# Optimization experiments

Measured on AMD Instinct MI355X. Metric: run time of the kernel, lower is better.

Reference implementation:

```python
import jax, jax.numpy as jnp
import numpy as np

B, N, F, K = 16384, 64, 128, 64


def setup_inputs() -> dict:
    key = jax.random.key(0)
    kx, kd = jax.random.split(key)
    x = jax.random.normal(kx, (B, F), dtype=jnp.float32)
    D = jax.random.normal(kd, (N, F, K), dtype=jnp.float32)  # per-cluster factor dictionaries
    return {"x": x, "D": D}


def reference(x, D):
    # --- assignment step (torch.no_grad in original) ---
    # Dtx[n,b,j] = sum_i D[n,i,j] * x[b,i]
    Dtx = jnp.einsum('nij,bi->nbj', D, x)                      # [N,B,K]
    # per-cluster (D^T D)^{-1}, batched inverse over the cluster axis
    DTD = jnp.einsum('nij,nik->njk', D, D)                     # [N,K,K]
    DTD_inv = jnp.linalg.inv(DTD)                              # [N,K,K]
    Cs = jnp.einsum('nbj,nkj->nbk', Dtx, DTD_inv)              # [N,B,K]
    x_hat = jnp.einsum('nij,nbj->nbi', D, Cs)                  # [N,B,F]
    # nearest-subspace assignment per sample
    label = jnp.argmin(jnp.linalg.norm(x_hat - x[None], axis=-1), axis=0)  # [B] int
    C = Cs[label, jnp.arange(x.shape[0])]                      # [B,K] gather per sample
    # --- reconstruction loss: sum_i || x[i] - D[label[i]] @ C[i] ||^2 ---
    x_rec = jnp.einsum('bik,bk->bi', D[label], C)              # grouped gather + matmul
    se_loss = jnp.sum(jnp.square(x - x_rec))
    return se_loss, label
```

## Files before the change

### kernel.cpp

```cpp
#include <hip/hip_runtime.h>
#include <hip/hip_bf16.h>

#define B_N 16384
#define TAU 0.25f
#define GS 68
#define YS 133

typedef float f32x4 __attribute__((ext_vector_type(4)));
typedef short s16x8 __attribute__((ext_vector_type(8)));

__device__ __forceinline__ void gl_lds16(const void* g, void* l) {
    __builtin_amdgcn_global_load_lds(
        (const __attribute__((address_space(1))) void*)g,
        (__attribute__((address_space(3))) void*)l, 16, 0, 0);
}

__device__ __forceinline__ unsigned short bf16_bits(float v) {
    __hip_bfloat16 h = __float2bfloat16(v);
    return *reinterpret_cast<unsigned short*>(&h);
}

__global__ __launch_bounds__(256) void prep_convert(const float* __restrict__ x,
                                                    const float* __restrict__ D,
                                                    unsigned short* __restrict__ xh,
                                                    float* __restrict__ nrm,
                                                    float* __restrict__ Qg,
                                                    unsigned short* __restrict__ Bht,
                                                    float* __restrict__ out) {
    const int t = threadIdx.x;

    if (blockIdx.x >= 64) {
        const int gid = (blockIdx.x - 64) * 256 + t;
        if (gid == 0) out[0] = 0.0f;
        const size_t base = (size_t)gid * 32;
        float s = 0.0f;
        #pragma unroll
        for (int c = 0; c < 8; ++c) {
            const f32x4 v = ((const f32x4*)(x + base))[c];
            s += v.x * v.x + v.y * v.y + v.z * v.z + v.w * v.w;
            ushort4 h;
            h.x = bf16_bits(v.x); h.y = bf16_bits(v.y);
            h.z = bf16_bits(v.z); h.w = bf16_bits(v.w);
            ((ushort4*)(xh + base))[c] = h;
        }
        s += __shfl_xor(s, 1, 64);
        s += __shfl_xor(s, 2, 64);
        if ((gid & 3) == 0) nrm[gid >> 2] = s;
        return;
    }

    __shared__ float Y[64 * YS];
    __shared__ __align__(16) float G[64 * GS + 64];
    __shared__ __align__(16) float Lti[8 * 8 * 8];
    const int n = blockIdx.x;
    const float* Dn = D + (size_t)n * 8192;

    for (int e4 = t; e4 < 2048; e4 += 256) {
        const int c = e4 >> 4, j4 = (e4 & 15) * 4;
        const f32x4 v = ((const f32x4*)Dn)[e4];
        Y[(j4 + 0) * YS + c] = v.x;
        Y[(j4 + 1) * YS + c] = v.y;
        Y[(j4 + 2) * YS + c] = v.z;
        Y[(j4 + 3) * YS + c] = v.w;
    }

    {
        const int a0 = (t & 15) * 4, b0 = (t >> 4) * 4;
        float acc[4][4] = {};
        #pragma unroll 4
        for (int i = 0; i < 128; ++i) {
            const f32x4 av = *(const f32x4*)(Dn + i * 64 + a0);
            const f32x4 bv = *(const f32x4*)(Dn + i * 64 + b0);
            const float aa[4] = {av.x, av.y, av.z, av.w};
            const float bb[4] = {bv.x, bv.y, bv.z, bv.w};
            #pragma unroll
            for (int p = 0; p < 4; ++p)
                #pragma unroll
                for (int q = 0; q < 4; ++q) acc[p][q] = fmaf(aa[p], bb[q], acc[p][q]);
        }
        #pragma unroll
        for (int p = 0; p < 4; ++p)
            #pragma unroll
            for (int q = 0; q < 4; ++q) G[(a0 + p) * GS + b0 + q] = acc[p][q];
    }
    __syncthreads();

    for (int p8 = 0; p8 < 8; ++p8) {
        const int pb = p8 * 8;
        if (t < 64) {
            const int lane = t;
            const f32x4 v0 = *(const f32x4*)&G[lane * GS + pb];
            const f32x4 v1 = *(const f32x4*)&G[lane * GS + pb + 4];
            float g[8] = {v0.x, v0.y, v0.z, v0.w, v1.x, v1.y, v1.z, v1.w};
            #pragma unroll
            for (int kk = 0; kk < 8; ++kk) {
                const int k = pb + kk;
                const float dk = __shfl(g[kk], k, 64);
                const float rinv = 1.0f / sqrtf(dk);
                const float lik = g[kk] * rinv;
                g[kk] = lik;
                if (lane == 0) G[64 * GS + k] = rinv;
                #pragma unroll
                for (int jj = kk + 1; jj < 8; ++jj) {
                    const float ljk = __shfl(lik, pb + jj, 64);
                    g[jj] -= lik * ljk;
                }
            }
            *(f32x4*)&G[lane * GS + pb]     = (f32x4){g[0], g[1], g[2], g[3]};
            *(f32x4*)&G[lane * GS + pb + 4] = (f32x4){g[4], g[5], g[6], g[7]};
        }
        __syncthreads();
        const int base = pb + 8;
        if (base < 64) {
            for (int i = base + (t >> 5); i < 64; i += 8) {
                const f32x4 Li0 = *(const f32x4*)&G[i * GS + pb];
                const f32x4 Li1 = *(const f32x4*)&G[i * GS + pb + 4];
                for (int j = base + (t & 31); j < 64; j += 32) {
                    const f32x4 Lj0 = *(const f32x4*)&G[j * GS + pb];
                    const f32x4 Lj1 = *(const f32x4*)&G[j * GS + pb + 4];
                    float s = G[i * GS + j];
                    s -= Li0.x * Lj0.x + Li0.y * Lj0.y + Li0.z * Lj0.z + Li0.w * Lj0.w;
                    s -= Li1.x * Lj1.x + Li1.y * Lj1.y + Li1.z * Lj1.z + Li1.w * Lj1.w;
                    G[i * GS + j] = s;
                }
            }
        }
        __syncthreads();
    }

    if (t < 64) {
        const int bi = t >> 3, c = t & 7;
        const int base = bi * 8;
        float m[8];
        #pragma unroll
        for (int r = 0; r < 8; ++r) {
            float s = (r == c) ? 1.0f : 0.0f;
            #pragma unroll
            for (int k = 0; k < r; ++k)
                s -= G[(base + r) * GS + base + k] * m[k];
            m[r] = s * G[64 * GS + base + r];
        }
        #pragma unroll
        for (int r = 0; r < 8; ++r) Lti[(base + r) * 8 + c] = m[r];
    }
    __syncthreads();

    if (t < 128) {
        const int c = t;
        for (int i = 0; i < 8; ++i) {
            float Tv[8];
            #pragma unroll
            for (int r = 0; r < 8; ++r) Tv[r] = Y[(i * 8 + r) * YS + c];
            for (int k = 0; k < i; ++k) {
                #pragma unroll
                for (int kk = 0; kk < 8; ++kk) {
                    const float z = Y[(k * 8 + kk) * YS + c];
                    #pragma unroll
                    for (int r = 0; r < 8; ++r)
                        Tv[r] -= G[(i * 8 + r) * GS + k * 8 + kk] * z;
                }
            }
            #pragma unroll
            for (int r = 0; r < 8; ++r) {
                float z = 0.0f;
                #pragma unroll
                for (int rp = 0; rp <= r; ++rp)
                    z += Lti[(i * 8 + r) * 8 + rp] * Tv[rp];
                Y[(i * 8 + r) * YS + c] = z;
            }
        }
    }
    __syncthreads();

    for (int e = t; e < 8192; e += 256) {
        const int j = e >> 7, i = e & 127;
        Bht[((size_t)n * 64 + j) * 128 + i] = bf16_bits(Y[j * YS + i]);
    }
    for (int e = t; e < 8192; e += 256) {
        const int i = e >> 6, j = e & 63;
        Qg[(size_t)n * 8192 + e] = Y[j * YS + i];
    }
}

__global__ __launch_bounds__(256) void gemm_argmax(const unsigned short* __restrict__ xh,
                                                   const unsigned short* __restrict__ Bht,
                                                   const float* __restrict__ nrm,
                                                   const float* __restrict__ x,
                                                   const float* __restrict__ Qg,
                                                   float* __restrict__ out) {
    __shared__ __align__(16) unsigned short ldsA[64 * 128];
    __shared__ float scL[64 * 65];
    __shared__ float mrg[4][64][3];
    __shared__ int sflags[64];
    __shared__ int scnt;
    __shared__ float ssum;
    __shared__ float scorr[4];

    const int t = threadIdx.x, w = t >> 6, lane = t & 63;
    const int m0 = blockIdx.x * 64;
    const int lm = lane & 15, lg = lane >> 4;
    if (t == 0) scnt = 0;
    if (t < 4) scorr[t] = 0.0f;

    {
        const int rl = lane >> 4, sp = lane & 15;
        #pragma unroll
        for (int q = 0; q < 4; ++q) {
            const int row = w * 16 + q * 4 + rl;
            const int c = sp ^ (row & 15);
            gl_lds16(xh + (size_t)(m0 + row) * 128 + c * 8,
                     &ldsA[(w * 16 + q * 4) * 128]);
        }
    }
    __syncthreads();

    s16x8 bfr[4][4];
    #pragma unroll
    for (int st = 0; st < 4; ++st) {
        const int r = st * 16 + lm;
        #pragma unroll
        for (int ks = 0; ks < 4; ++ks) {
            const int p = (ks * 4 + lg) ^ (r & 15);
            bfr[st][ks] = *(const s16x8*)&ldsA[r * 128 + p * 8];
        }
    }

    float v1[4] = {-1e30f, -1e30f, -1e30f, -1e30f};
    float v2[4] = {-1e30f, -1e30f, -1e30f, -1e30f};
    int   n1[4] = {0, 0, 0, 0};

    const unsigned short* afbase = Bht + (size_t)lm * 128 + lg * 8;

#define LOAD_AF(dst, cc) do {                                                   \
    const unsigned short* bp = afbase + (size_t)(cc) * 8192;                    \
    _Pragma("unroll")                                                           \
    for (int mt_ = 0; mt_ < 4; ++mt_)                                           \
        _Pragma("unroll")                                                       \
        for (int ks_ = 0; ks_ < 4; ++ks_)                                       \
            dst[mt_][ks_] = *(const s16x8*)(bp + mt_ * 2048 + ks_ * 32);        \
} while (0)

#define PROC(af, cc) do {                                                       \
    _Pragma("unroll")                                                           \
    for (int st_ = 0; st_ < 4; ++st_) {                                         \
        f32x4 ac0 = {0.f,0.f,0.f,0.f}, ac1 = {0.f,0.f,0.f,0.f};                 \
        f32x4 ac2 = {0.f,0.f,0.f,0.f}, ac3 = {0.f,0.f,0.f,0.f};                 \
        _Pragma("unroll")                                                       \
        for (int ks_ = 0; ks_ < 4; ++ks_) {                                     \
            ac0 = __builtin_amdgcn_mfma_f32_16x16x32_bf16(af[0][ks_], bfr[st_][ks_], ac0, 0, 0, 0); \
            ac1 = __builtin_amdgcn_mfma_f32_16x16x32_bf16(af[1][ks_], bfr[st_][ks_], ac1, 0, 0, 0); \
            ac2 = __builtin_amdgcn_mfma_f32_16x16x32_bf16(af[2][ks_], bfr[st_][ks_], ac2, 0, 0, 0); \
            ac3 = __builtin_amdgcn_mfma_f32_16x16x32_bf16(af[3][ks_], bfr[st_][ks_], ac3, 0, 0, 0); \
        }                                                                       \
        float q0 = ac0[0]*ac0[0]; q0 = fmaf(ac0[1],ac0[1],q0);                  \
        q0 = fmaf(ac0[2],ac0[2],q0); q0 = fmaf(ac0[3],ac0[3],q0);               \
        float q1 = ac1[0]*ac1[0]; q1 = fmaf(ac1[1],ac1[1],q1);                  \
        q1 = fmaf(ac1[2],ac1[2],q1); q1 = fmaf(ac1[3],ac1[3],q1);               \
        float q2 = ac2[0]*ac2[0]; q2 = fmaf(ac2[1],ac2[1],q2);                  \
        q2 = fmaf(ac2[2],ac2[2],q2); q2 = fmaf(ac2[3],ac2[3],q2);               \
        float q3 = ac3[0]*ac3[0]; q3 = fmaf(ac3[1],ac3[1],q3);                  \
        q3 = fmaf(ac3[2],ac3[2],q3); q3 = fmaf(ac3[3],ac3[3],q3);               \
        float s_ = ((q0 + q1) + q2) + q3;                                       \
        s_ += __shfl_xor(s_, 16, 64);                                           \
        s_ += __shfl_xor(s_, 32, 64);                                           \
        if (lg == 0) scL[(st_ * 16 + lm) * 65 + (cc)] = s_;                     \
        if (s_ > v1[st_]) { v2[st_] = v1[st_]; v1[st_] = s_; n1[st_] = (cc); }  \
        else v2[st_] = fmaxf(v2[st_], s_);                                      \
    }                                                                           \
} while (0)

    {
        const int cb = w * 16;
        s16x8 afA[4][4], afB[4][4];
        LOAD_AF(afA, cb);
        #pragma unroll 1
        for (int ci = 0; ci < 16; ci += 2) {
            LOAD_AF(afB, cb + ci + 1);
            PROC(afA, cb + ci);
            if (ci < 14) LOAD_AF(afA, cb + ci + 2);
            PROC(afB, cb + ci + 1);
        }
    }
#undef LOAD_AF
#undef PROC

    if (lg == 0) {
        #pragma unroll
        for (int st = 0; st < 4; ++st) {
            mrg[w][st * 16 + lm][0] = v1[st];
            mrg[w][st * 16 + lm][1] = v2[st];
            mrg[w][st * 16 + lm][2] = (float)n1[st];
        }
    }
    __syncthreads();

    if (t < 64) {
        float b1 = -1e30f, b2 = -1e30f;
        int bn = 0;
        #pragma unroll
        for (int ww = 0; ww < 4; ++ww) {
            const float a1 = mrg[ww][t][0];
            const float a2 = mrg[ww][t][1];
            const int an = (int)mrg[ww][t][2];
            if (a1 > b1) { b2 = fmaxf(b1, a2); b1 = a1; bn = an; }
            else b2 = fmaxf(b2, a1);
        }
        out[1 + m0 + t] = (float)bn;
        if (b1 - b2 < TAU) { const int i = atomicAdd(&scnt, 1); sflags[i] = t; }
        float err = nrm[m0 + t] - b1;
        err += __shfl_xor(err, 1, 64);
        err += __shfl_xor(err, 2, 64);
        err += __shfl_xor(err, 4, 64);
        err += __shfl_xor(err, 8, 64);
        err += __shfl_xor(err, 16, 64);
        err += __shfl_xor(err, 32, 64);
        if (t == 0) ssum = err;
    }
    __syncthreads();

    const int nf = scnt;
    float corr = 0.0f;
    for (int f = w; f < nf; f += 4) {
        const int s = sflags[f];
        const int b2 = m0 + s;
        const float v = scL[s * 65 + lane];
        float vm = v;
        for (int off = 32; off; off >>= 1) vm = fmaxf(vm, __shfl_xor(vm, off, 64));
        unsigned long long mask = __ballot((vm - v) < TAU);
        float best = -1e30f;
        int bn = 0;
        while (mask) {
            const int nn = (int)__builtin_ctzll(mask);
            mask &= mask - 1;
            const float* Qn = Qg + (size_t)nn * 8192;
            const float* xb = x + (size_t)b2 * 128;
            float d0 = 0.0f, d1 = 0.0f, d2 = 0.0f, d3 = 0.0f;
            #pragma unroll
            for (int i = 0; i < 128; i += 4) {
                d0 = fmaf(Qn[(i + 0) * 64 + lane], xb[i + 0], d0);
                d1 = fmaf(Qn[(i + 1) * 64 + lane], xb[i + 1], d1);
                d2 = fmaf(Qn[(i + 2) * 64 + lane], xb[i + 2], d2);
                d3 = fmaf(Qn[(i + 3) * 64 + lane], xb[i + 3], d3);
            }
            const float dot = (d0 + d1) + (d2 + d3);
            float sv = dot * dot;
            for (int off = 32; off; off >>= 1) sv += __shfl_xor(sv, off, 64);
            if (sv > best) { best = sv; bn = nn; }
        }
        if (lane == 0) {
            out[1 + b2] = (float)bn;
            corr += vm - best;
        }
    }
    if (lane == 0 && corr != 0.0f) scorr[w] += corr;
    __syncthreads();
    if (t == 0)
        atomicAdd(out, ssum + scorr[0] + scorr[1] + scorr[2] + scorr[3]);
}

extern "C" void kernel_launch(void* const* d_in, const int* in_sizes, int n_in,
                              void* d_out, int out_size, void* d_ws, size_t ws_size,
                              hipStream_t stream) {
    const float* x = (const float*)d_in[0];
    const float* D = (const float*)d_in[1];
    float* out = (float*)d_out;

    char* ws = (char*)d_ws;
    unsigned short* xh  = (unsigned short*)(ws);
    unsigned short* Bht = (unsigned short*)(ws + (4u << 20));
    float* Qg           = (float*)(ws + (5u << 20));
    float* nrm          = (float*)(ws + (11u << 20));

    prep_convert<<<320, 256, 0, stream>>>(x, D, xh, nrm, Qg, Bht, out);
    gemm_argmax<<<256, 256, 0, stream>>>(xh, Bht, nrm, x, Qg, out);
}
```

Measured before the change: 149.3 us.

## Shrink gemm_argmax tile to 16 rows per block and launch 1024 blocks

Cuts the per-block sample tile from 64 to 16 rows and launches four times as many blocks. The goal is to fill all CUs (256 blocks underfill a 256-CU part with one block each) and to lower register and LDS use so more waves can be resident. It also drops the explicit double-buffered prefetch of the B fragments. In exchange, each B fragment loaded from global/L2 is reused across only 16 rows instead of 64, which quadruples B traffic, and there is more per-block overhead including more atomics on the output.

```diff
diff --git a/kernel.cpp b/kernel.cpp
--- a/kernel.cpp
+++ b/kernel.cpp
@@ -182,119 +182,91 @@
     }
 }
 
-__global__ __launch_bounds__(256) void gemm_argmax(const unsigned short* __restrict__ xh,
-                                                   const unsigned short* __restrict__ Bht,
-                                                   const float* __restrict__ nrm,
-                                                   const float* __restrict__ x,
-                                                   const float* __restrict__ Qg,
-                                                   float* __restrict__ out) {
-    __shared__ __align__(16) unsigned short ldsA[64 * 128];
-    __shared__ float scL[64 * 65];
-    __shared__ float mrg[4][64][3];
-    __shared__ int sflags[64];
+__global__ __launch_bounds__(256, 4) void gemm_argmax(const unsigned short* __restrict__ xh,
+                                                      const unsigned short* __restrict__ Bht,
+                                                      const float* __restrict__ nrm,
+                                                      const float* __restrict__ x,
+                                                      const float* __restrict__ Qg,
+                                                      float* __restrict__ out) {
+    __shared__ __align__(16) unsigned short ldsA[16 * 128];
+    __shared__ float scL[16 * 65];
+    __shared__ float mrg[4][16][3];
+    __shared__ int sflags[16];
     __shared__ int scnt;
     __shared__ float ssum;
     __shared__ float scorr[4];
 
     const int t = threadIdx.x, w = t >> 6, lane = t & 63;
-    const int m0 = blockIdx.x * 64;
+    const int m0 = blockIdx.x * 16;
     const int lm = lane & 15, lg = lane >> 4;
     if (t == 0) scnt = 0;
     if (t < 4) scorr[t] = 0.0f;
 
     {
         const int rl = lane >> 4, sp = lane & 15;
-        #pragma unroll
-        for (int q = 0; q < 4; ++q) {
-            const int row = w * 16 + q * 4 + rl;
-            const int c = sp ^ (row & 15);
-            gl_lds16(xh + (size_t)(m0 + row) * 128 + c * 8,
-                     &ldsA[(w * 16 + q * 4) * 128]);
-        }
-    }
-    __syncthreads();
-
-    s16x8 bfr[4][4];
+        const int row = w * 4 + rl;
+        const int c = sp ^ (row & 15);
+        gl_lds16(xh + (size_t)(m0 + row) * 128 + c * 8, &ldsA[(w * 4) * 128]);
+    }
+    __syncthreads();
+
+    s16x8 bfr[4];
     #pragma unroll
-    for (int st = 0; st < 4; ++st) {
-        const int r = st * 16 + lm;
+    for (int ks = 0; ks < 4; ++ks) {
+        const int p = (ks * 4 + lg) ^ (lm & 15);
+        bfr[ks] = *(const s16x8*)&ldsA[lm * 128 + p * 8];
+    }
+
+    float v1 = -1e30f, v2 = -1e30f;
+    int n1 = 0;
+
+    const unsigned short* afbase = Bht + (size_t)lm * 128 + lg * 8;
+
+    #pragma unroll 1
+    for (int ci = 0; ci < 16; ++ci) {
+        const int cc = w * 16 + ci;
+        const unsigned short* bp = afbase + (size_t)cc * 8192;
+
+        s16x8 af[4][4];
+        #pragma unroll
+        for (int mt = 0; mt < 4; ++mt)
+            #pragma unroll
+            for (int ks = 0; ks < 4; ++ks)
+                af[mt][ks] = *(const s16x8*)(bp + mt * 2048 + ks * 32);
+
+        f32x4 ac0 = {0.f,0.f,0.f,0.f}, ac1 = {0.f,0.f,0.f,0.f};
+        f32x4 ac2 = {0.f,0.f,0.f,0.f}, ac3 = {0.f,0.f,0.f,0.f};
         #pragma unroll
         for (int ks = 0; ks < 4; ++ks) {
-            const int p = (ks * 4 + lg) ^ (r & 15);
-            bfr[st][ks] = *(const s16x8*)&ldsA[r * 128 + p * 8];
-        }
-    }
-
-    float v1[4] = {-1e30f, -1e30f, -1e30f, -1e30f};
-    float v2[4] = {-1e30f, -1e30f, -1e30f, -1e30f};
-    int   n1[4] = {0, 0, 0, 0};
-
-    const unsigned short* afbase = Bht + (size_t)lm * 128 + lg * 8;
-
-#define LOAD_AF(dst, cc) do {                                                   \
-    const unsigned short* bp = afbase + (size_t)(cc) * 8192;                    \
-    _Pragma("unroll")                                                           \
-    for (int mt_ = 0; mt_ < 4; ++mt_)                                           \
-        _Pragma("unroll")                                                       \
-        for (int ks_ = 0; ks_ < 4; ++ks_)                                       \
-            dst[mt_][ks_] = *(const s16x8*)(bp + mt_ * 2048 + ks_ * 32);        \
-} while (0)
-
-#define PROC(af, cc) do {                                                       \
-    _Pragma("unroll")                                                           \
-    for (int st_ = 0; st_ < 4; ++st_) {                                         \
-        f32x4 ac0 = {0.f,0.f,0.f,0.f}, ac1 = {0.f,0.f,0.f,0.f};                 \
-        f32x4 ac2 = {0.f,0.f,0.f,0.f}, ac3 = {0.f,0.f,0.f,0.f};                 \
-        _Pragma("unroll")                                                       \
-        for (int ks_ = 0; ks_ < 4; ++ks_) {                                     \
-            ac0 = __builtin_amdgcn_mfma_f32_16x16x32_bf16(af[0][ks_], bfr[st_][ks_], ac0, 0, 0, 0); \
-            ac1 = __builtin_amdgcn_mfma_f32_16x16x32_bf16(af[1][ks_], bfr[st_][ks_], ac1, 0, 0, 0); \
-            ac2 = __builtin_amdgcn_mfma_f32_16x16x32_bf16(af[2][ks_], bfr[st_][ks_], ac2, 0, 0, 0); \
-            ac3 = __builtin_amdgcn_mfma_f32_16x16x32_bf16(af[3][ks_], bfr[st_][ks_], ac3, 0, 0, 0); \
-        }                                                                       \
-        float q0 = ac0[0]*ac0[0]; q0 = fmaf(ac0[1],ac0[1],q0);                  \
-        q0 = fmaf(ac0[2],ac0[2],q0); q0 = fmaf(ac0[3],ac0[3],q0);               \
-        float q1 = ac1[0]*ac1[0]; q1 = fmaf(ac1[1],ac1[1],q1);                  \
-        q1 = fmaf(ac1[2],ac1[2],q1); q1 = fmaf(ac1[3],ac1[3],q1);               \
-        float q2 = ac2[0]*ac2[0]; q2 = fmaf(ac2[1],ac2[1],q2);                  \
-        q2 = fmaf(ac2[2],ac2[2],q2); q2 = fmaf(ac2[3],ac2[3],q2);               \
-        float q3 = ac3[0]*ac3[0]; q3 = fmaf(ac3[1],ac3[1],q3);                  \
-        q3 = fmaf(ac3[2],ac3[2],q3); q3 = fmaf(ac3[3],ac3[3],q3);               \
-        float s_ = ((q0 + q1) + q2) + q3;                                       \
-        s_ += __shfl_xor(s_, 16, 64);                                           \
-        s_ += __shfl_xor(s_, 32, 64);                                           \
-        if (lg == 0) scL[(st_ * 16 + lm) * 65 + (cc)] = s_;                     \
-        if (s_ > v1[st_]) { v2[st_] = v1[st_]; v1[st_] = s_; n1[st_] = (cc); }  \
-        else v2[st_] = fmaxf(v2[st_], s_);                                      \
-    }                                                                           \
-} while (0)
-
-    {
-        const int cb = w * 16;
-        s16x8 afA[4][4], afB[4][4];
-        LOAD_AF(afA, cb);
-        #pragma unroll 1
-        for (int ci = 0; ci < 16; ci += 2) {
-            LOAD_AF(afB, cb + ci + 1);
-            PROC(afA, cb + ci);
-            if (ci < 14) LOAD_AF(afA, cb + ci + 2);
-            PROC(afB, cb + ci + 1);
-        }
-    }
-#undef LOAD_AF
-#undef PROC
+            ac0 = __builtin_amdgcn_mfma_f32_16x16x32_bf16(af[0][ks], bfr[ks], ac0, 0, 0, 0);
+            ac1 = __builtin_amdgcn_mfma_f32_16x16x32_bf16(af[1][ks], bfr[ks], ac1, 0, 0, 0);
+            ac2 = __builtin_amdgcn_mfma_f32_16x16x32_bf16(af[2][ks], bfr[ks], ac2, 0, 0, 0);
+            ac3 = __builtin_amdgcn_mfma_f32_16x16x32_bf16(af[3][ks], bfr[ks], ac3, 0, 0, 0);
+        }
+        float q0 = ac0[0]*ac0[0]; q0 = fmaf(ac0[1],ac0[1],q0);
+        q0 = fmaf(ac0[2],ac0[2],q0); q0 = fmaf(ac0[3],ac0[3],q0);
+        float q1 = ac1[0]*ac1[0]; q1 = fmaf(ac1[1],ac1[1],q1);
+        q1 = fmaf(ac1[2],ac1[2],q1); q1 = fmaf(ac1[3],ac1[3],q1);
+        float q2 = ac2[0]*ac2[0]; q2 = fmaf(ac2[1],ac2[1],q2);
+        q2 = fmaf(ac2[2],ac2[2],q2); q2 = fmaf(ac2[3],ac2[3],q2);
+        float q3 = ac3[0]*ac3[0]; q3 = fmaf(ac3[1],ac3[1],q3);
+        q3 = fmaf(ac3[2],ac3[2],q3); q3 = fmaf(ac3[3],ac3[3],q3);
+        float s_ = ((q0 + q1) + q2) + q3;
+        s_ += __shfl_xor(s_, 16, 64);
+        s_ += __shfl_xor(s_, 32, 64);
+        if (lg == 0) scL[lm * 65 + cc] = s_;
+        if (s_ > v1) { v2 = v1; v1 = s_; n1 = cc; }
+        else v2 = fmaxf(v2, s_);
+    }
 
     if (lg == 0) {
-        #pragma unroll
-        for (int st = 0; st < 4; ++st) {
-            mrg[w][st * 16 + lm][0] = v1[st];
-            mrg[w][st * 16 + lm][1] = v2[st];
-            mrg[w][st * 16 + lm][2] = (float)n1[st];
-        }
-    }
-    __syncthreads();
-
-    if (t < 64) {
+        mrg[w][lm][0] = v1;
+        mrg[w][lm][1] = v2;
+        mrg[w][lm][2] = (float)n1;
+    }
+    __syncthreads();
+
+    if (t < 16) {
         float b1 = -1e30f, b2 = -1e30f;
         int bn = 0;
         #pragma unroll
@@ -312,8 +284,6 @@
         err += __shfl_xor(err, 2, 64);
         err += __shfl_xor(err, 4, 64);
         err += __shfl_xor(err, 8, 64);
-        err += __shfl_xor(err, 16, 64);
-        err += __shfl_xor(err, 32, 64);
         if (t == 0) ssum = err;
     }
     __syncthreads();
@@ -372,5 +342,5 @@
     float* nrm          = (float*)(ws + (11u << 20));
 
     prep_convert<<<320, 256, 0, stream>>>(x, D, xh, nrm, Qg, Bht, out);
-    gemm_argmax<<<256, 256, 0, stream>>>(xh, Bht, nrm, x, Qg, out);
-}
+    gemm_argmax<<<1024, 256, 0, stream>>>(xh, Bht, nrm, x, Qg, out);
+}
```

Measured after the change: 283.7 us. 90.1% more time.
